# Kernel tuning notes

Measured on AMD Instinct MI355X. Metric: run time of the kernel, lower is better.

The kernel has to match this reference:

```python
import jax, jax.numpy as jnp
import numpy as np

BATCH = 8192
IN_DIM = 2048
OUT_DIM = 2048
DEPTH = 5


def setup_inputs() -> dict:
    key = jax.random.key(0)
    k1, k2, k3, k4 = jax.random.split(key, 4)
    x = jax.random.normal(k1, (BATCH, IN_DIM), dtype=jnp.float32)
    hyperdimensional_weights = jax.random.normal(k2, (DEPTH, IN_DIM, OUT_DIM), dtype=jnp.float32)
    classical_weights = jax.random.normal(k3, (IN_DIM, OUT_DIM), dtype=jnp.float32)
    classical_biases = jax.random.normal(k4, (OUT_DIM,), dtype=jnp.float32)
    return {
        "x": x,
        "hyperdimensional_weights": hyperdimensional_weights,
        "classical_weights": classical_weights,
        "classical_biases": classical_biases,
    }


def _hyperdimensional_probs(hd_w):
    # angle = W[d, j, 0], phase = W[d, j, 1] for output index j (j < input_dims)
    depth, in_dim, _ = hd_w.shape
    angles = hd_w[:, :OUT_DIM, 0]   # [depth, out]
    phases = hd_w[:, :OUT_DIM, 1]   # [depth, out]
    # Initial uniform state 1/sqrt(n), replicated per output unit j.
    s0 = jnp.full((OUT_DIM, in_dim), 1.0 / np.sqrt(in_dim), dtype=jnp.complex64)

    def step(s, ang_ph):
        ang, ph = ang_ph                      # each [out]
        c = jnp.cos(ang)[:, None]
        sn = jnp.sin(ang)[:, None]
        # Circulant rotation: new[k] = cos*s[k] - sin*s[k+1] + sin*s[k-1] (cyclic)
        s = c * s - sn * jnp.roll(s, -1, axis=1) + sn * jnp.roll(s, 1, axis=1)
        # Global phase gate: diag(e^{i*phase})
        s = s * jnp.exp(1j * ph)[:, None]
        return s, None

    s, _ = jax.lax.scan(step, s0, (angles, phases))
    # probability = |state[0]|^2
    return jnp.abs(s[:, 0]) ** 2              # [out], real float32


def reference(x, hyperdimensional_weights, classical_weights, classical_biases):
    classical = x @ classical_weights + classical_biases            # [B, out]
    hd = _hyperdimensional_probs(hyperdimensional_weights)          # [out] (batch-independent)
    return jnp.tanh(classical + hd[None, :])
```

## Files before the change

### kernel.cpp

```cpp
#include <hip/hip_runtime.h>

#define BATCH 8192
#define DIM   2048
#define DEPTH 5


#define BUFSZ  49152
#define ABYTES 32768

typedef short bf16x8_t __attribute__((ext_vector_type(8)));
typedef float f32x4_t  __attribute__((ext_vector_type(4)));

__device__ __forceinline__ unsigned short f2bf(float f) {
  unsigned u = __float_as_uint(f);
  u += 0x7fffu + ((u >> 16) & 1u);
  return (unsigned short)(u >> 16);
}
__device__ __forceinline__ float bf2f(unsigned short h) {
  return __uint_as_float(((unsigned)h) << 16);
}

__global__ void prep_fused_kernel(const float* __restrict__ x,
                                  const float* __restrict__ hdw,
                                  const float* __restrict__ W,
                                  const float* __restrict__ bias,
                                  float* __restrict__ bias2,
                                  unsigned short* __restrict__ xhi,
                                  unsigned short* __restrict__ xlo,
                                  unsigned short* __restrict__ whi,
                                  unsigned short* __restrict__ wlo) {
  __shared__ float tile[32][33];
  const int b = blockIdx.x;
  const int tid = threadIdx.x;

  if (b < 8192) {
    size_t g = (size_t)b * 256 + tid;
    const float4* xp = (const float4*)(x + g * 8);
    float4 v0 = xp[0], v1 = xp[1];
    float v[8] = {v0.x, v0.y, v0.z, v0.w, v1.x, v1.y, v1.z, v1.w};
    bf16x8_t h, lo;
#pragma unroll
    for (int j = 0; j < 8; ++j) {
      unsigned short hj = f2bf(v[j]);
      h[j] = (short)hj;
      lo[j] = (short)f2bf(v[j] - bf2f(hj));
    }
    ((bf16x8_t*)xhi)[g] = h;
    ((bf16x8_t*)xlo)[g] = lo;
  } else if (b < 12288) {
    const int t = b - 8192;
    const int k0 = (t >> 6) * 32;
    const int n0 = (t & 63) * 32;
    const int tx = tid & 31;
    const int ty = tid >> 5;
#pragma unroll
    for (int r = 0; r < 32; r += 8)
      tile[ty + r][tx] = W[(size_t)(k0 + ty + r) * DIM + n0 + tx];
    __syncthreads();
    const int n = tid >> 3;
    const int kq = (tid & 7) * 4;
    ushort4 hv, lv;
    float vv0 = tile[kq + 0][n], vv1 = tile[kq + 1][n];
    float vv2 = tile[kq + 2][n], vv3 = tile[kq + 3][n];
    hv.x = f2bf(vv0); lv.x = f2bf(vv0 - bf2f(hv.x));
    hv.y = f2bf(vv1); lv.y = f2bf(vv1 - bf2f(hv.y));
    hv.z = f2bf(vv2); lv.z = f2bf(vv2 - bf2f(hv.z));
    hv.w = f2bf(vv3); lv.w = f2bf(vv3 - bf2f(hv.w));
    const size_t o = (size_t)(n0 + n) * DIM + k0 + kq;
    *(ushort4*)(whi + o) = hv;
    *(ushort4*)(wlo + o) = lv;
  } else {
    int j = (b - 12288) * 256 + tid;
    float p = 1.0f;
#pragma unroll
    for (int d = 0; d < DEPTH; ++d)
      p *= cosf(hdw[(size_t)d * DIM * DIM + (size_t)j * DIM]);
    bias2[j] = bias[j] + p * p * (1.0f / 2048.0f);
  }
}

#define GLDS(SRC, OFF)                                                         \
  __builtin_amdgcn_global_load_lds(                                            \
      (const __attribute__((address_space(1))) unsigned int*)(SRC),            \
      (__attribute__((address_space(3))) unsigned int*)(smem + (OFF)), 16, 0, 0)

#define MFMA16(A, B, C) __builtin_amdgcn_mfma_f32_16x16x32_bf16((A), (B), (C), 0, 0, 0)

__global__ __launch_bounds__(512, 2) void gemm_pipe_kernel(
    const unsigned short* __restrict__ Ah, const unsigned short* __restrict__ Al,
    const unsigned short* __restrict__ Bh, const unsigned short* __restrict__ Bl,
    const float* __restrict__ bias2, float* __restrict__ out) {
  __shared__ float4 smem4[3 * BUFSZ / 16];
  char* smem = (char*)smem4;

  const int tid  = threadIdx.x;
  const int lane = tid & 63;
  const int wave = tid >> 6;
  const int wm   = wave >> 1;
  const int wn   = wave & 1;
  const int l15  = lane & 15;
  const int kl   = lane >> 4;
  const int bm = blockIdx.x;
  const int bn = blockIdx.y;

  const int rsub = wave * 16 + (lane >> 2);
  const int kg   = ((lane & 3) ^ ((lane >> 3) & 3)) * 8;
  const unsigned short* sA0 = Ah + ((size_t)(bm * 256 +       rsub)) * DIM + kg;
  const unsigned short* sA1 = Ah + ((size_t)(bm * 256 + 128 + rsub)) * DIM + kg;
  const unsigned short* sA2 = Al + ((size_t)(bm * 256 +       rsub)) * DIM + kg;
  const unsigned short* sA3 = Al + ((size_t)(bm * 256 + 128 + rsub)) * DIM + kg;
  const unsigned short* sB0 = Bh + ((size_t)(bn * 128 +       rsub)) * DIM + kg;
  const unsigned short* sB1 = Bl + ((size_t)(bn * 128 +       rsub)) * DIM + kg;
  const unsigned wdst = wave * 1024;

  const int foff = l15 * 64 + ((kl * 16) ^ (((l15 >> 1) & 3) << 4));

  const f32x4_t vzero = {0.f, 0.f, 0.f, 0.f};
  f32x4_t acc[4][4];
#pragma unroll
  for (int i = 0; i < 4; ++i)
#pragma unroll
    for (int j = 0; j < 4; ++j) acc[i][j] = vzero;

  GLDS(sA0,      0             + wdst);
  GLDS(sA1,      8192          + wdst);
  GLDS(sB0,      ABYTES        + wdst);
  GLDS(sA2,      16384         + wdst);
  GLDS(sA3,      24576         + wdst);
  GLDS(sB1,      ABYTES + 8192 + wdst);
  GLDS(sA0 + 32, BUFSZ + 0             + wdst);
  GLDS(sA1 + 32, BUFSZ + 8192          + wdst);
  GLDS(sB0 + 32, BUFSZ + ABYTES        + wdst);
  GLDS(sA2 + 32, BUFSZ + 16384         + wdst);
  GLDS(sA3 + 32, BUFSZ + 24576         + wdst);
  GLDS(sB1 + 32, BUFSZ + ABYTES + 8192 + wdst);

  asm volatile("s_waitcnt vmcnt(6)" ::: "memory");
  asm volatile("s_barrier" ::: "memory");

#pragma unroll 1
  for (int t = 0; t < 64; ++t) {
    const unsigned bo = (unsigned)(t % 3) * BUFSZ;
    const unsigned so = (unsigned)((t + 2) % 3) * BUFSZ;
    const int ko = (t + 2) * 32;

    if (t < 62) {
      GLDS(sA0 + ko, so + 0             + wdst);
      GLDS(sA1 + ko, so + 8192          + wdst);
      GLDS(sB0 + ko, so + ABYTES        + wdst);
      GLDS(sA2 + ko, so + 16384         + wdst);
      GLDS(sA3 + ko, so + 24576         + wdst);
      GLDS(sB1 + ko, so + ABYTES + 8192 + wdst);
    }

    bf16x8_t bh[4], bl[4], ah[2], al[2];
    const char* pB = smem + bo + ABYTES + wn * 4096 + foff;
#pragma unroll
    for (int nt = 0; nt < 4; ++nt) {
      bh[nt] = *(const bf16x8_t*)(pB + nt * 1024);
      bl[nt] = *(const bf16x8_t*)(pB + 8192 + nt * 1024);
    }
    const char* pA = smem + bo + wm * 4096 + foff;
    ah[0] = *(const bf16x8_t*)(pA);
    al[0] = *(const bf16x8_t*)(pA + 16384);
    ah[1] = *(const bf16x8_t*)(pA + 1024);
    al[1] = *(const bf16x8_t*)(pA + 16384 + 1024);

    __builtin_amdgcn_s_setprio(1);
#pragma unroll
    for (int i = 0; i < 2; ++i)
#pragma unroll
      for (int nt = 0; nt < 4; ++nt) {
        acc[i][nt] = MFMA16(ah[i], bh[nt], acc[i][nt]);
        acc[i][nt] = MFMA16(ah[i], bl[nt], acc[i][nt]);
        acc[i][nt] = MFMA16(al[i], bh[nt], acc[i][nt]);
      }
    __builtin_amdgcn_s_setprio(0);

    bf16x8_t ah2[2], al2[2];
    ah2[0] = *(const bf16x8_t*)(pA + 2048);
    al2[0] = *(const bf16x8_t*)(pA + 16384 + 2048);
    ah2[1] = *(const bf16x8_t*)(pA + 3072);
    al2[1] = *(const bf16x8_t*)(pA + 16384 + 3072);

    __builtin_amdgcn_s_setprio(1);
#pragma unroll
    for (int i = 0; i < 2; ++i)
#pragma unroll
      for (int nt = 0; nt < 4; ++nt) {
        acc[2 + i][nt] = MFMA16(ah2[i], bh[nt], acc[2 + i][nt]);
        acc[2 + i][nt] = MFMA16(ah2[i], bl[nt], acc[2 + i][nt]);
        acc[2 + i][nt] = MFMA16(al2[i], bh[nt], acc[2 + i][nt]);
      }
    __builtin_amdgcn_s_setprio(0);

    if (t < 62)       { asm volatile("s_waitcnt vmcnt(6)" ::: "memory"); }
    else if (t == 62) { asm volatile("s_waitcnt vmcnt(0)" ::: "memory"); }
    if (t < 63)       { asm volatile("s_barrier" ::: "memory"); }
  }

  const int orow0 = bm * 256 + wm * 64;
  const int ocol0 = bn * 128 + wn * 64;
#pragma unroll
  for (int j = 0; j < 4; ++j) {
    const int col = ocol0 + j * 16 + l15;
    const float b2 = bias2[col];
#pragma unroll
    for (int i = 0; i < 4; ++i) {
      const int row = orow0 + i * 16 + kl * 4;
#pragma unroll
      for (int r = 0; r < 4; ++r) {
        float z = acc[i][j][r] + b2;
        float e = __expf(2.0f * z);
        out[(size_t)(row + r) * DIM + col] = 1.0f - 2.0f / (e + 1.0f);
      }
    }
  }
}

extern "C" void kernel_launch(void* const* d_in, const int* in_sizes, int n_in,
                              void* d_out, int out_size, void* d_ws, size_t ws_size,
                              hipStream_t stream) {
  const float* x   = (const float*)d_in[0];
  const float* hdw = (const float*)d_in[1];
  const float* W   = (const float*)d_in[2];
  const float* b   = (const float*)d_in[3];
  float* out = (float*)d_out;

  char* ws = (char*)d_ws;
  unsigned short* xhi  = (unsigned short*)ws;
  unsigned short* xlo  = xhi + (size_t)BATCH * DIM;
  unsigned short* wThi = xlo + (size_t)BATCH * DIM;
  unsigned short* wTlo = wThi + (size_t)DIM * DIM;
  float*          bias2 = (float*)(wTlo + (size_t)DIM * DIM);

  prep_fused_kernel<<<12296, 256, 0, stream>>>(
      x, hdw, W, b, bias2, xhi, xlo, wThi, wTlo);
  gemm_pipe_kernel<<<dim3(BATCH / 256, DIM / 128), 512, 0, stream>>>(
      xhi, xlo, wThi, wTlo, bias2, out);
}
```

Before: 355.8 us.

## Enlarge GEMM block tile to 256x256 with double-buffered LDS

Widens each workgroup's output tile from 256x128 to 256x256, so each wave holds a 64x128 accumulator block (32 f32x4 accumulators). The pipeline changes from triple buffering with two stages in flight to double buffering with one stage in flight, and it waits with vmcnt(0) every iteration. The aim is more MFMA reuse per LDS load and less global traffic per output element. In exchange it uses more registers, which may cut occupancy at 2 blocks per CU or cause spills, and it leaves less latency hiding for the loads. The grid shrinks to 256 blocks, which may underfill the 256 CUs.

```diff
diff --git a/kernel.cpp b/kernel.cpp
--- a/kernel.cpp
+++ b/kernel.cpp
@@ -5,7 +5,7 @@
 #define DEPTH 5
 
 
-#define BUFSZ  49152
+#define BUFSZ  65536
 #define ABYTES 32768
 
 typedef short bf16x8_t __attribute__((ext_vector_type(8)));
@@ -86,11 +86,23 @@
 
 #define MFMA16(A, B, C) __builtin_amdgcn_mfma_f32_16x16x32_bf16((A), (B), (C), 0, 0, 0)
 
+#define STAGE(KO, SO)                                                          \
+  do {                                                                         \
+    GLDS(sAh + (KO),             (SO) + 0              + wdst);                \
+    GLDS(sAh + 128 * DIM + (KO), (SO) + 8192           + wdst);                \
+    GLDS(sAl + (KO),             (SO) + 16384          + wdst);                \
+    GLDS(sAl + 128 * DIM + (KO), (SO) + 24576          + wdst);                \
+    GLDS(sBh + (KO),             (SO) + ABYTES + 0     + wdst);                \
+    GLDS(sBh + 128 * DIM + (KO), (SO) + ABYTES + 8192  + wdst);                \
+    GLDS(sBl + (KO),             (SO) + ABYTES + 16384 + wdst);                \
+    GLDS(sBl + 128 * DIM + (KO), (SO) + ABYTES + 24576 + wdst);                \
+  } while (0)
+
 __global__ __launch_bounds__(512, 2) void gemm_pipe_kernel(
     const unsigned short* __restrict__ Ah, const unsigned short* __restrict__ Al,
     const unsigned short* __restrict__ Bh, const unsigned short* __restrict__ Bl,
     const float* __restrict__ bias2, float* __restrict__ out) {
-  __shared__ float4 smem4[3 * BUFSZ / 16];
+  __shared__ float4 smem4[2 * BUFSZ / 16];
   char* smem = (char*)smem4;
 
   const int tid  = threadIdx.x;
@@ -105,112 +117,101 @@
 
   const int rsub = wave * 16 + (lane >> 2);
   const int kg   = ((lane & 3) ^ ((lane >> 3) & 3)) * 8;
-  const unsigned short* sA0 = Ah + ((size_t)(bm * 256 +       rsub)) * DIM + kg;
-  const unsigned short* sA1 = Ah + ((size_t)(bm * 256 + 128 + rsub)) * DIM + kg;
-  const unsigned short* sA2 = Al + ((size_t)(bm * 256 +       rsub)) * DIM + kg;
-  const unsigned short* sA3 = Al + ((size_t)(bm * 256 + 128 + rsub)) * DIM + kg;
-  const unsigned short* sB0 = Bh + ((size_t)(bn * 128 +       rsub)) * DIM + kg;
-  const unsigned short* sB1 = Bl + ((size_t)(bn * 128 +       rsub)) * DIM + kg;
+  const unsigned short* sAh = Ah + ((size_t)(bm * 256 + rsub)) * DIM + kg;
+  const unsigned short* sAl = Al + ((size_t)(bm * 256 + rsub)) * DIM + kg;
+  const unsigned short* sBh = Bh + ((size_t)(bn * 256 + rsub)) * DIM + kg;
+  const unsigned short* sBl = Bl + ((size_t)(bn * 256 + rsub)) * DIM + kg;
   const unsigned wdst = wave * 1024;
 
   const int foff = l15 * 64 + ((kl * 16) ^ (((l15 >> 1) & 3) << 4));
 
   const f32x4_t vzero = {0.f, 0.f, 0.f, 0.f};
-  f32x4_t acc[4][4];
+  f32x4_t acc[4][8];
 #pragma unroll
   for (int i = 0; i < 4; ++i)
 #pragma unroll
-    for (int j = 0; j < 4; ++j) acc[i][j] = vzero;
-
-  GLDS(sA0,      0             + wdst);
-  GLDS(sA1,      8192          + wdst);
-  GLDS(sB0,      ABYTES        + wdst);
-  GLDS(sA2,      16384         + wdst);
-  GLDS(sA3,      24576         + wdst);
-  GLDS(sB1,      ABYTES + 8192 + wdst);
-  GLDS(sA0 + 32, BUFSZ + 0             + wdst);
-  GLDS(sA1 + 32, BUFSZ + 8192          + wdst);
-  GLDS(sB0 + 32, BUFSZ + ABYTES        + wdst);
-  GLDS(sA2 + 32, BUFSZ + 16384         + wdst);
-  GLDS(sA3 + 32, BUFSZ + 24576         + wdst);
-  GLDS(sB1 + 32, BUFSZ + ABYTES + 8192 + wdst);
-
-  asm volatile("s_waitcnt vmcnt(6)" ::: "memory");
+    for (int j = 0; j < 8; ++j) acc[i][j] = vzero;
+
+  STAGE(0, 0);
+  asm volatile("s_waitcnt vmcnt(0)" ::: "memory");
   asm volatile("s_barrier" ::: "memory");
 
 #pragma unroll 1
   for (int t = 0; t < 64; ++t) {
-    const unsigned bo = (unsigned)(t % 3) * BUFSZ;
-    const unsigned so = (unsigned)((t + 2) % 3) * BUFSZ;
-    const int ko = (t + 2) * 32;
-
-    if (t < 62) {
-      GLDS(sA0 + ko, so + 0             + wdst);
-      GLDS(sA1 + ko, so + 8192          + wdst);
-      GLDS(sB0 + ko, so + ABYTES        + wdst);
-      GLDS(sA2 + ko, so + 16384         + wdst);
-      GLDS(sA3 + ko, so + 24576         + wdst);
-      GLDS(sB1 + ko, so + ABYTES + 8192 + wdst);
-    }
-
-    bf16x8_t bh[4], bl[4], ah[2], al[2];
-    const char* pB = smem + bo + ABYTES + wn * 4096 + foff;
-#pragma unroll
-    for (int nt = 0; nt < 4; ++nt) {
-      bh[nt] = *(const bf16x8_t*)(pB + nt * 1024);
-      bl[nt] = *(const bf16x8_t*)(pB + 8192 + nt * 1024);
-    }
+    const unsigned bo = (unsigned)(t & 1) * BUFSZ;
+    const unsigned so = bo ^ BUFSZ;
+
+    if (t < 63) {
+      const int ko = (t + 1) * 32;
+      STAGE(ko, so);
+    }
+
     const char* pA = smem + bo + wm * 4096 + foff;
-    ah[0] = *(const bf16x8_t*)(pA);
-    al[0] = *(const bf16x8_t*)(pA + 16384);
-    ah[1] = *(const bf16x8_t*)(pA + 1024);
-    al[1] = *(const bf16x8_t*)(pA + 16384 + 1024);
-
-    __builtin_amdgcn_s_setprio(1);
-#pragma unroll
-    for (int i = 0; i < 2; ++i)
+    bf16x8_t ah[4], al[4];
+#pragma unroll
+    for (int mt = 0; mt < 4; ++mt) {
+      ah[mt] = *(const bf16x8_t*)(pA + mt * 1024);
+      al[mt] = *(const bf16x8_t*)(pA + 16384 + mt * 1024);
+    }
+
+    const char* pB = smem + bo + ABYTES + wn * 8192 + foff;
+
+    {
+      bf16x8_t bh[4], bl[4];
 #pragma unroll
       for (int nt = 0; nt < 4; ++nt) {
-        acc[i][nt] = MFMA16(ah[i], bh[nt], acc[i][nt]);
-        acc[i][nt] = MFMA16(ah[i], bl[nt], acc[i][nt]);
-        acc[i][nt] = MFMA16(al[i], bh[nt], acc[i][nt]);
+        bh[nt] = *(const bf16x8_t*)(pB + nt * 1024);
+        bl[nt] = *(const bf16x8_t*)(pB + 16384 + nt * 1024);
       }
-    __builtin_amdgcn_s_setprio(0);
-
-    bf16x8_t ah2[2], al2[2];
-    ah2[0] = *(const bf16x8_t*)(pA + 2048);
-    al2[0] = *(const bf16x8_t*)(pA + 16384 + 2048);
-    ah2[1] = *(const bf16x8_t*)(pA + 3072);
-    al2[1] = *(const bf16x8_t*)(pA + 16384 + 3072);
-
-    __builtin_amdgcn_s_setprio(1);
-#pragma unroll
-    for (int i = 0; i < 2; ++i)
+      __builtin_amdgcn_s_setprio(1);
+#pragma unroll
+      for (int mt = 0; mt < 4; ++mt)
+#pragma unroll
+        for (int nt = 0; nt < 4; ++nt) {
+          acc[mt][nt] = MFMA16(ah[mt], bh[nt], acc[mt][nt]);
+          acc[mt][nt] = MFMA16(ah[mt], bl[nt], acc[mt][nt]);
+          acc[mt][nt] = MFMA16(al[mt], bh[nt], acc[mt][nt]);
+        }
+      __builtin_amdgcn_s_setprio(0);
+    }
+
+    {
+      bf16x8_t bh[4], bl[4];
 #pragma unroll
       for (int nt = 0; nt < 4; ++nt) {
-        acc[2 + i][nt] = MFMA16(ah2[i], bh[nt], acc[2 + i][nt]);
-        acc[2 + i][nt] = MFMA16(ah2[i], bl[nt], acc[2 + i][nt]);
-        acc[2 + i][nt] = MFMA16(al2[i], bh[nt], acc[2 + i][nt]);
+        bh[nt] = *(const bf16x8_t*)(pB + 4096 + nt * 1024);
+        bl[nt] = *(const bf16x8_t*)(pB + 16384 + 4096 + nt * 1024);
       }
-    __builtin_amdgcn_s_setprio(0);
-
-    if (t < 62)       { asm volatile("s_waitcnt vmcnt(6)" ::: "memory"); }
-    else if (t == 62) { asm volatile("s_waitcnt vmcnt(0)" ::: "memory"); }
-    if (t < 63)       { asm volatile("s_barrier" ::: "memory"); }
+      __builtin_amdgcn_s_setprio(1);
+#pragma unroll
+      for (int mt = 0; mt < 4; ++mt)
+#pragma unroll
+        for (int nt = 0; nt < 4; ++nt) {
+          acc[mt][4 + nt] = MFMA16(ah[mt], bh[nt], acc[mt][4 + nt]);
+          acc[mt][4 + nt] = MFMA16(ah[mt], bl[nt], acc[mt][4 + nt]);
+          acc[mt][4 + nt] = MFMA16(al[mt], bh[nt], acc[mt][4 + nt]);
+        }
+      __builtin_amdgcn_s_setprio(0);
+    }
+
+    if (t < 63) {
+      asm volatile("s_waitcnt vmcnt(0)" ::: "memory");
+      asm volatile("s_barrier" ::: "memory");
+    }
   }
 
   const int orow0 = bm * 256 + wm * 64;
-  const int ocol0 = bn * 128 + wn * 64;
-#pragma unroll
-  for (int j = 0; j < 4; ++j) {
-    const int col = ocol0 + j * 16 + l15;
+  const int ocol0 = bn * 256 + wn * 128;
+#pragma unroll
+  for (int nt = 0; nt < 8; ++nt) {
+    const int col = ocol0 + nt * 16 + l15;
     const float b2 = bias2[col];
 #pragma unroll
-    for (int i = 0; i < 4; ++i) {
-      const int row = orow0 + i * 16 + kl * 4;
+    for (int mt = 0; mt < 4; ++mt) {
+      const int row = orow0 + mt * 16 + kl * 4;
 #pragma unroll
       for (int r = 0; r < 4; ++r) {
-        float z = acc[i][j][r] + b2;
+        float z = acc[mt][nt][r] + b2;
         float e = __expf(2.0f * z);
         out[(size_t)(row + r) * DIM + col] = 1.0f - 2.0f / (e + 1.0f);
       }
@@ -236,6 +237,6 @@
 
   prep_fused_kernel<<<12296, 256, 0, stream>>>(
       x, hdw, W, b, bias2, xhi, xlo, wThi, wTlo);
-  gemm_pipe_kernel<<<dim3(BATCH / 256, DIM / 128), 512, 0, stream>>>(
+  gemm_pipe_kernel<<<dim3(BATCH / 256, DIM / 256), 512, 0, stream>>>(
       xhi, xlo, wThi, wTlo, bias2, out);
 }
```

New measurement: 333.8 us. 6.2% less time.
